# Kernel optimization log

Measured on AMD Instinct MI355X. Metric: run time of the kernel, lower is better.

Reference implementation:

```python
import jax, jax.numpy as jnp
import numpy as np

ALIGN_CORNERS = True   # module init arg
NUM_AUX = 8            # auxiliary samples for linearized multi-sampling
NOISE_STRENGTH = 0.5   # noise scale in units of input pixel spacing
EPS = 1e-6             # Tikhonov term for the per-pixel 2x2 least squares


def _base_coords(n, align_corners):
    if align_corners:
        return jnp.linspace(-1.0, 1.0, n, dtype=jnp.float32)
    return (jnp.arange(n, dtype=jnp.float32) * 2.0 + 1.0) / n - 1.0


def affine_grid(theta, h_out, w_out, align_corners):
    # theta: [B,2,3] -> grid [B,h_out,w_out,2] with (x,y) in [-1,1]
    xs = _base_coords(w_out, align_corners)
    ys = _base_coords(h_out, align_corners)
    X, Y = jnp.meshgrid(xs, ys)                      # [H,W]
    base = jnp.stack([X, Y, jnp.ones_like(X)], -1)   # [H,W,3]
    return jnp.einsum('hwk,bik->bhwi', base, theta)  # [B,H,W,2]


def bilinear_sample(image, grid, align_corners):
    # image [B,C,Hi,Wi], grid [B,H,W,2] -> [B,H,W,C], zero padding outside
    B, C, Hi, Wi = image.shape
    x, y = grid[..., 0], grid[..., 1]
    if align_corners:
        ix = (x + 1.0) * 0.5 * (Wi - 1)
        iy = (y + 1.0) * 0.5 * (Hi - 1)
    else:
        ix = ((x + 1.0) * Wi - 1.0) * 0.5
        iy = ((y + 1.0) * Hi - 1.0) * 0.5
    x0 = jnp.floor(ix); y0 = jnp.floor(iy)
    wx1 = ix - x0; wy1 = iy - y0
    bidx = jnp.arange(B)[:, None, None]

    def tap(xi, yi, w):
        valid = (xi >= 0) & (xi <= Wi - 1) & (yi >= 0) & (yi <= Hi - 1)
        xc = jnp.clip(xi, 0, Wi - 1).astype(jnp.int32)
        yc = jnp.clip(yi, 0, Hi - 1).astype(jnp.int32)
        v = image[bidx, :, yc, xc]                   # [B,H,W,C] gather
        return v * (w * valid)[..., None]

    return (tap(x0, y0, (1 - wx1) * (1 - wy1)) +
            tap(x0 + 1, y0, wx1 * (1 - wy1)) +
            tap(x0, y0 + 1, (1 - wx1) * wy1) +
            tap(x0 + 1, y0 + 1, wx1 * wy1))


def linearized_grid_sample(image, grid, align_corners):
    # Linearized multi-sampling (Jiang et al., ICCV'19): forward value equals
    # the center bilinear sample; gradient wrt grid flows through a per-pixel
    # least-squares linearization fitted from NUM_AUX noisy auxiliary samples.
    B, C, Hi, Wi = image.shape
    key = jax.random.key(42)
    spacing = jnp.array([2.0 / Wi, 2.0 / Hi], dtype=jnp.float32)  # one input pixel in norm coords
    g0 = jax.lax.stop_gradient(grid)
    noise = jax.random.normal(key, (B, NUM_AUX) + grid.shape[1:3] + (2,), dtype=jnp.float32)
    aux = g0[:, None] + noise * NOISE_STRENGTH * spacing          # [B,K,H,W,2]

    center = bilinear_sample(image, g0, align_corners)            # [B,H,W,C]
    samp = jax.vmap(lambda g: bilinear_sample(image, g, align_corners),
                    in_axes=1, out_axes=1)(aux)                   # [B,K,H,W,C]

    d_int = samp - center[:, None]                                # [B,K,H,W,C]
    d_grid = aux - g0[:, None]                                    # [B,K,H,W,2]
    xtx = jnp.einsum('bkhwi,bkhwj->bhwij', d_grid, d_grid) \
        + EPS * jnp.eye(2, dtype=jnp.float32)                     # [B,H,W,2,2]
    xty = jnp.einsum('bkhwi,bkhwc->bhwic', d_grid, d_int)         # [B,H,W,2,C]
    slope = jnp.linalg.solve(xtx, xty)                            # [B,H,W,2,C]

    out = center + jnp.einsum('bhwic,bhwi->bhwc', slope, grid - g0)
    return jnp.transpose(out, (0, 3, 1, 2))                       # [B,C,H,W]


def setup_inputs() -> dict:
    key = jax.random.key(0)
    k1, k2 = jax.random.split(key)
    B, C, Hi, Wi = 4, 3, 1024, 1024
    image = jax.random.normal(k1, (B, C, Hi, Wi), dtype=jnp.float32)
    ident = jnp.tile(jnp.array([[1.0, 0.0, 0.0], [0.0, 1.0, 0.0]], dtype=jnp.float32), (B, 1, 1))
    pMtrx = ident + 0.05 * jax.random.normal(k2, (B, 2, 3), dtype=jnp.float32)
    return {"image": image, "pMtrx": pMtrx, "W": 1024, "H": 1024}


def reference(image, pMtrx, W, H):
    # torch.affine_grid_generator(pMtrx, (B,3,W,H)) -> grid [B, W, H, 2]
    grid = affine_grid(pMtrx, W, H, ALIGN_CORNERS)
    return linearized_grid_sample(image, grid, ALIGN_CORNERS)  # [B,C,W,H]
```

## Files before the change

### kernel.cpp

```cpp
#include <hip/hip_runtime.h>


#define B_  4
#define C_  3
#define HI  1024
#define WI  1024
#define HO  1024
#define WO  1024

#define TW  64
#define TH  32
#define MAXSEG  22
#define MAXROWS 48

typedef __attribute__((address_space(3))) void* lds_vp;
typedef const __attribute__((address_space(1))) void* gbl_vp;
typedef float f32x4 __attribute__((ext_vector_type(4)));

__device__ __forceinline__ float2 map_px(int w, int h,
                                         float t0, float t1, float t2,
                                         float t3, float t4, float t5) {
    const float xs = -1.0f + 2.0f * (float)w / (float)(WO - 1);
    const float ys = -1.0f + 2.0f * (float)h / (float)(HO - 1);
    const float x = t0 * xs + (t1 * ys + t2);
    const float y = t3 * xs + (t4 * ys + t5);
    const float ix = (x + 1.0f) * 0.5f * (float)(WI - 1);
    const float iy = (y + 1.0f) * 0.5f * (float)(HI - 1);
    return make_float2(ix, iy);
}

__global__ __launch_bounds__(256) void warp_bilinear_fast_kernel(
    const float* __restrict__ image,
    const float* __restrict__ theta,
    float* __restrict__ out)
{
    __shared__ float lds[MAXSEG * 4 * MAXROWS * C_];

    const int bid = blockIdx.x;
    const int sid = ((bid & 7) << 8) | (bid >> 3);

    const int b   = sid >> 9;
    const int rem = sid & 511;
    const int h0  = (rem >> 4) * TH;
    const int w0  = (rem & 15) * TW;

    const float* t = theta + b * 6;
    const float t0 = t[0], t1 = t[1], t2 = t[2];
    const float t3 = t[3], t4 = t[4], t5 = t[5];

    const float2 c00 = map_px(w0,        h0,        t0,t1,t2,t3,t4,t5);
    const float2 c10 = map_px(w0+TW-1,   h0,        t0,t1,t2,t3,t4,t5);
    const float2 c01 = map_px(w0,        h0+TH-1,   t0,t1,t2,t3,t4,t5);
    const float2 c11 = map_px(w0+TW-1,   h0+TH-1,   t0,t1,t2,t3,t4,t5);

    const float ixmin = fminf(fminf(c00.x, c10.x), fminf(c01.x, c11.x));
    const float iymin = fminf(fminf(c00.y, c10.y), fminf(c01.y, c11.y));
    const float ixmax = fmaxf(fmaxf(c00.x, c10.x), fmaxf(c01.x, c11.x));
    const float iymax = fmaxf(fmaxf(c00.y, c10.y), fmaxf(c01.y, c11.y));

    int xlo = (int)floorf(ixmin) - 1;
    int xhi = (int)floorf(ixmax) + 2;
    xlo = min(max(xlo, 0), WI - 1);
    xhi = min(max(xhi, xlo), WI - 1);
    int bx = xlo & ~3;
    const int nseg = min((xhi - bx + 4) >> 2, MAXSEG);
    bx = min(bx, WI - 4 * nseg);

    int ylo = (int)floorf(iymin) - 1;
    int yhi = (int)floorf(iymax) + 2;
    ylo = min(max(ylo, 0), HI - 1);
    yhi = min(max(yhi, ylo), HI - 1);
    const int nrows = min(yhi - ylo + 1, MAXROWS);
    const int by = min(ylo, HI - nrows);

    const int rowf   = nseg << 2;
    const int segch  = nrows * nseg;
    const int segtot = C_ * segch;
    const int chf    = segch << 2;

    const float rcp_segch = 1.0f / (float)segch;
    const float rcp_nseg  = 1.0f / (float)nseg;

    const float* imgb = image + (size_t)b * (C_ * HI * WI);

    const int wv   = threadIdx.x >> 6;
    const int lane = threadIdx.x & 63;
    const int niter = (segtot + 63) >> 6;
    for (int j = wv; j < niter; j += 4) {
        const int seg = (j << 6) + lane;
        if (seg < segtot) {
            const int c  = (int)(((float)seg + 0.5f) * rcp_segch);
            const int r2 = seg - c * segch;
            const int r  = (int)(((float)r2 + 0.5f) * rcp_nseg);
            const int s  = r2 - r * nseg;
            const float* gp = imgb + c * (HI * WI) + (by + r) * WI + (bx + (s << 2));
            __builtin_amdgcn_global_load_lds((gbl_vp)gp, (lds_vp)(lds + (j << 8)),
                                             16, 0, 0);
        }
    }
    __syncthreads();

    const int qx  = threadIdx.x & 15;
    const int rr  = threadIdx.x >> 4;
    const int wq  = w0 + (qx << 2);

    float* ob = out + (size_t)b * (C_ * HO * WO) + wq;

    const bool interior = (ixmin >= 1.0f) && (ixmax <= (float)(WI - 2)) &&
                          (iymin >= 1.0f) && (iymax <= (float)(HI - 2));

#pragma unroll
    for (int rh = 0; rh < 2; ++rh) {
        const int h = h0 + rr + (rh << 4);

        const float ys = -1.0f + 2.0f * (float)h / (float)(HO - 1);
        const float xb = t1 * ys + t2;
        const float yb = t4 * ys + t5;

        float o0[4], o1[4], o2[4];

        if (interior) {
#pragma unroll
            for (int px = 0; px < 4; ++px) {
                const int w = wq + px;
                const float xs = -1.0f + 2.0f * (float)w / (float)(WO - 1);
                const float x = t0 * xs + xb;
                const float y = t3 * xs + yb;
                const float ix = (x + 1.0f) * 0.5f * (float)(WI - 1);
                const float iy = (y + 1.0f) * 0.5f * (float)(HI - 1);

                const float x0f = floorf(ix);
                const float y0f = floorf(iy);
                const float wx1 = ix - x0f;
                const float wy1 = iy - y0f;
                const float wx0 = 1.0f - wx1;
                const float wy0 = 1.0f - wy1;

                const float w00 = wx0 * wy0, w10 = wx1 * wy0;
                const float w01 = wx0 * wy1, w11 = wx1 * wy1;

                const int ox = (int)x0f - bx;
                const int oy = (int)y0f - by;
                const float* base0 = lds + oy * rowf + ox;

                {
                    const float* p = base0;
                    o0[px] = p[0]    * w00 + p[1]        * w10
                           + p[rowf] * w01 + p[rowf + 1] * w11;
                }
                {
                    const float* p = base0 + chf;
                    o1[px] = p[0]    * w00 + p[1]        * w10
                           + p[rowf] * w01 + p[rowf + 1] * w11;
                }
                {
                    const float* p = base0 + 2 * chf;
                    o2[px] = p[0]    * w00 + p[1]        * w10
                           + p[rowf] * w01 + p[rowf + 1] * w11;
                }
            }
        } else {
#pragma unroll
            for (int px = 0; px < 4; ++px) {
                const int w = wq + px;
                const float xs = -1.0f + 2.0f * (float)w / (float)(WO - 1);
                const float x = t0 * xs + xb;
                const float y = t3 * xs + yb;
                const float ix = (x + 1.0f) * 0.5f * (float)(WI - 1);
                const float iy = (y + 1.0f) * 0.5f * (float)(HI - 1);

                const float x0f = floorf(ix);
                const float y0f = floorf(iy);
                const float wx1 = ix - x0f;
                const float wy1 = iy - y0f;
                const int x0 = (int)x0f;
                const int y0 = (int)y0f;

                const float ax0 = (1.0f - wx1) * ((x0 >= 0 && x0 <= WI - 1) ? 1.0f : 0.0f);
                const float ax1 = wx1          * ((x0 >= -1 && x0 <= WI - 2) ? 1.0f : 0.0f);
                const float ay0 = (1.0f - wy1) * ((y0 >= 0 && y0 <= HI - 1) ? 1.0f : 0.0f);
                const float ay1 = wy1          * ((y0 >= -1 && y0 <= HI - 2) ? 1.0f : 0.0f);

                const float w00 = ax0 * ay0, w10 = ax1 * ay0;
                const float w01 = ax0 * ay1, w11 = ax1 * ay1;

                const int bw = (nseg << 2) - 1;
                const int xl0 = min(max(min(max(x0,     0), WI - 1) - bx, 0), bw);
                const int xl1 = min(max(min(max(x0 + 1, 0), WI - 1) - bx, 0), bw);
                const int yl0 = min(max(min(max(y0,     0), HI - 1) - by, 0), nrows - 1);
                const int yl1 = min(max(min(max(y0 + 1, 0), HI - 1) - by, 0), nrows - 1);

                const int o00 = yl0 * rowf + xl0;
                const int o10 = yl0 * rowf + xl1;
                const int o01 = yl1 * rowf + xl0;
                const int o11 = yl1 * rowf + xl1;

                o0[px] = lds[o00] * w00 + lds[o10] * w10
                       + lds[o01] * w01 + lds[o11] * w11;
                o1[px] = lds[chf + o00] * w00 + lds[chf + o10] * w10
                       + lds[chf + o01] * w01 + lds[chf + o11] * w11;
                o2[px] = lds[2*chf + o00] * w00 + lds[2*chf + o10] * w10
                       + lds[2*chf + o01] * w01 + lds[2*chf + o11] * w11;
            }
        }

        f32x4 s0 = { o0[0], o0[1], o0[2], o0[3] };
        f32x4 s1 = { o1[0], o1[1], o1[2], o1[3] };
        f32x4 s2 = { o2[0], o2[1], o2[2], o2[3] };
        float* obr = ob + (size_t)h * WO;
        __builtin_nontemporal_store(s0, (f32x4*)(obr));
        __builtin_nontemporal_store(s1, (f32x4*)(obr + (size_t)(HO * WO)));
        __builtin_nontemporal_store(s2, (f32x4*)(obr + (size_t)(2 * HO * WO)));
    }
}

extern "C" void kernel_launch(void* const* d_in, const int* in_sizes, int n_in,
                              void* d_out, int out_size, void* d_ws, size_t ws_size,
                              hipStream_t stream) {
    const float* image = (const float*)d_in[0];
    const float* theta = (const float*)d_in[1];
    float* out = (float*)d_out;

    const int grid = B_ * (HO / TH) * (WO / TW);
    warp_bilinear_fast_kernel<<<grid, 256, 0, stream>>>(image, theta, out);
}
```

Baseline: 107.9 us.

## Split work per channel so each block stages one channel in LDS

Each block now handles a single channel of a tile instead of all three. The grid grows threefold, and the LDS footprint per block drops to one third. The launch bound now requests 8 blocks per CU, aiming for higher occupancy and better latency hiding of the global-to-LDS loads. The cost is that per-tile coordinate and bounding-box setup is repeated for each channel, and there are more blocks to schedule.

```diff
diff --git a/kernel.cpp b/kernel.cpp
--- a/kernel.cpp
+++ b/kernel.cpp
@@ -29,20 +29,22 @@
     return make_float2(ix, iy);
 }
 
-__global__ __launch_bounds__(256) void warp_bilinear_fast_kernel(
+__global__ __launch_bounds__(256, 8) void warp_bilinear_fast_kernel(
     const float* __restrict__ image,
     const float* __restrict__ theta,
     float* __restrict__ out)
 {
-    __shared__ float lds[MAXSEG * 4 * MAXROWS * C_];
+    __shared__ float lds[MAXSEG * 4 * MAXROWS];
 
     const int bid = blockIdx.x;
-    const int sid = ((bid & 7) << 8) | (bid >> 3);
+    const int sid = (bid & 7) * 768 + (bid >> 3);
 
-    const int b   = sid >> 9;
-    const int rem = sid & 511;
-    const int h0  = (rem >> 4) * TH;
-    const int w0  = (rem & 15) * TW;
+    const int b    = sid / 1536;
+    const int r1   = sid - b * 1536;
+    const int c    = r1 >> 9;
+    const int tile = r1 & 511;
+    const int h0   = (tile >> 4) * TH;
+    const int w0   = (tile & 15) * TW;
 
     const float* t = theta + b * 6;
     const float t0 = t[0], t1 = t[1], t2 = t[2];
@@ -73,27 +75,22 @@
     const int nrows = min(yhi - ylo + 1, MAXROWS);
     const int by = min(ylo, HI - nrows);
 
-    const int rowf   = nseg << 2;
-    const int segch  = nrows * nseg;
-    const int segtot = C_ * segch;
-    const int chf    = segch << 2;
+    const int rowf  = nseg << 2;
+    const int segch = nrows * nseg;
 
-    const float rcp_segch = 1.0f / (float)segch;
-    const float rcp_nseg  = 1.0f / (float)nseg;
+    const float rcp_nseg = 1.0f / (float)nseg;
 
-    const float* imgb = image + (size_t)b * (C_ * HI * WI);
+    const float* imgc = image + (size_t)b * (C_ * HI * WI) + (size_t)c * (HI * WI);
 
     const int wv   = threadIdx.x >> 6;
     const int lane = threadIdx.x & 63;
-    const int niter = (segtot + 63) >> 6;
+    const int niter = (segch + 63) >> 6;
     for (int j = wv; j < niter; j += 4) {
         const int seg = (j << 6) + lane;
-        if (seg < segtot) {
-            const int c  = (int)(((float)seg + 0.5f) * rcp_segch);
-            const int r2 = seg - c * segch;
-            const int r  = (int)(((float)r2 + 0.5f) * rcp_nseg);
-            const int s  = r2 - r * nseg;
-            const float* gp = imgb + c * (HI * WI) + (by + r) * WI + (bx + (s << 2));
+        if (seg < segch) {
+            const int r = (int)(((float)seg + 0.5f) * rcp_nseg);
+            const int s = seg - r * nseg;
+            const float* gp = imgc + (by + r) * WI + (bx + (s << 2));
             __builtin_amdgcn_global_load_lds((gbl_vp)gp, (lds_vp)(lds + (j << 8)),
                                              16, 0, 0);
         }
@@ -104,7 +101,7 @@
     const int rr  = threadIdx.x >> 4;
     const int wq  = w0 + (qx << 2);
 
-    float* ob = out + (size_t)b * (C_ * HO * WO) + wq;
+    float* ob = out + (size_t)b * (C_ * HO * WO) + (size_t)c * (HO * WO) + wq;
 
     const bool interior = (ixmin >= 1.0f) && (ixmax <= (float)(WI - 2)) &&
                           (iymin >= 1.0f) && (iymax <= (float)(HI - 2));
@@ -117,7 +114,7 @@
         const float xb = t1 * ys + t2;
         const float yb = t4 * ys + t5;
 
-        float o0[4], o1[4], o2[4];
+        float o0[4];
 
         if (interior) {
 #pragma unroll
@@ -141,23 +138,10 @@
 
                 const int ox = (int)x0f - bx;
                 const int oy = (int)y0f - by;
-                const float* base0 = lds + oy * rowf + ox;
+                const float* p = lds + oy * rowf + ox;
 
-                {
-                    const float* p = base0;
-                    o0[px] = p[0]    * w00 + p[1]        * w10
-                           + p[rowf] * w01 + p[rowf + 1] * w11;
-                }
-                {
-                    const float* p = base0 + chf;
-                    o1[px] = p[0]    * w00 + p[1]        * w10
-                           + p[rowf] * w01 + p[rowf + 1] * w11;
-                }
-                {
-                    const float* p = base0 + 2 * chf;
-                    o2[px] = p[0]    * w00 + p[1]        * w10
-                           + p[rowf] * w01 + p[rowf + 1] * w11;
-                }
+                o0[px] = p[0]    * w00 + p[1]        * w10
+                       + p[rowf] * w01 + p[rowf + 1] * w11;
             }
         } else {
 #pragma unroll
@@ -190,27 +174,13 @@
                 const int yl0 = min(max(min(max(y0,     0), HI - 1) - by, 0), nrows - 1);
                 const int yl1 = min(max(min(max(y0 + 1, 0), HI - 1) - by, 0), nrows - 1);
 
-                const int o00 = yl0 * rowf + xl0;
-                const int o10 = yl0 * rowf + xl1;
-                const int o01 = yl1 * rowf + xl0;
-                const int o11 = yl1 * rowf + xl1;
-
-                o0[px] = lds[o00] * w00 + lds[o10] * w10
-                       + lds[o01] * w01 + lds[o11] * w11;
-                o1[px] = lds[chf + o00] * w00 + lds[chf + o10] * w10
-                       + lds[chf + o01] * w01 + lds[chf + o11] * w11;
-                o2[px] = lds[2*chf + o00] * w00 + lds[2*chf + o10] * w10
-                       + lds[2*chf + o01] * w01 + lds[2*chf + o11] * w11;
+                o0[px] = lds[yl0 * rowf + xl0] * w00 + lds[yl0 * rowf + xl1] * w10
+                       + lds[yl1 * rowf + xl0] * w01 + lds[yl1 * rowf + xl1] * w11;
             }
         }
 
         f32x4 s0 = { o0[0], o0[1], o0[2], o0[3] };
-        f32x4 s1 = { o1[0], o1[1], o1[2], o1[3] };
-        f32x4 s2 = { o2[0], o2[1], o2[2], o2[3] };
-        float* obr = ob + (size_t)h * WO;
-        __builtin_nontemporal_store(s0, (f32x4*)(obr));
-        __builtin_nontemporal_store(s1, (f32x4*)(obr + (size_t)(HO * WO)));
-        __builtin_nontemporal_store(s2, (f32x4*)(obr + (size_t)(2 * HO * WO)));
+        __builtin_nontemporal_store(s0, (f32x4*)(ob + (size_t)h * WO));
     }
 }
 
@@ -221,6 +191,6 @@
     const float* theta = (const float*)d_in[1];
     float* out = (float*)d_out;
 
-    const int grid = B_ * (HO / TH) * (WO / TW);
+    const int grid = B_ * C_ * (HO / TH) * (WO / TW);
     warp_bilinear_fast_kernel<<<grid, 256, 0, stream>>>(image, theta, out);
 }
```

After: 111.1 us. 1.03x slower.
